# Kernel optimization log

Hardware: AMD Instinct MI355X
Metric: run time of the kernel (lower is better)

The kernel has to match this reference:

```python
import jax, jax.numpy as jnp
import numpy as np

N_ATOMS = 50000
NUM_TYPES = 8
DIM_Q = 64
NUM_NEURONS = 64


def setup_inputs() -> dict:
    key = jax.random.key(0)
    k_q, k_z, k_w0, k_w1 = jax.random.split(key, 4)
    descriptors = jax.random.normal(k_q, (N_ATOMS, DIM_Q), dtype=jnp.float32)
    Z = jax.random.randint(k_z, (N_ATOMS,), 0, NUM_TYPES, dtype=jnp.int32)
    # glorot-ish scaled init for the per-type MLP weights
    W0 = jax.random.normal(k_w0, (NUM_TYPES, DIM_Q, NUM_NEURONS), dtype=jnp.float32) * np.float32(1.0 / np.sqrt(DIM_Q))
    b0 = jnp.zeros((NUM_TYPES, NUM_NEURONS), dtype=jnp.float32)
    W1 = jax.random.normal(k_w1, (NUM_TYPES, NUM_NEURONS), dtype=jnp.float32) * np.float32(1.0 / np.sqrt(NUM_NEURONS))
    b1 = jnp.zeros((), dtype=jnp.float32)
    return {"descriptors": descriptors, "W0": W0, "b0": b0, "W1": W1, "b1": b1, "Z": Z}


def reference(descriptors, W0, b0, W1, b1, Z):
    # Per-type gather of expert weights (the headroom hotspot):
    W0_t = W0[Z]          # [N, dim_q, num_neurons]
    b0_t = b0[Z]          # [N, num_neurons]
    W1_t = W1[Z]          # [N, num_neurons]
    # Batched 1-hidden-layer MLP per atom: h_i = tanh(q_i @ W0[Z_i] + b0[Z_i])
    h = jnp.tanh(jnp.einsum('nd,ndk->nk', descriptors, W0_t) + b0_t)  # [N, num_neurons]
    # Per-atom scalar energy, global bias b1, then total energy (target_mode == 0)
    E_i = jnp.sum(h * W1_t, axis=1) + b1  # [N]
    return jnp.sum(E_i)
```

## Files before the change

### kernel.cpp

```cpp
#include <hip/hip_runtime.h>
#include <math.h>

#define NUM_TYPES 8
#define DIM 64
#define SEG 8192
#define BM 128
#define QS_STRIDE 132

__global__ __launch_bounds__(256) void scatter_kernel(
    const int* __restrict__ Z, int* __restrict__ fill, int* __restrict__ sorted,
    const float* __restrict__ b1, float* __restrict__ out, int N)
{
    __shared__ int cnt[NUM_TYPES];
    __shared__ int base[NUM_TYPES];
    int tid = threadIdx.x;
    if (tid < NUM_TYPES) cnt[tid] = 0;
    __syncthreads();

    int i = blockIdx.x * 256 + tid;
    int z = 0, r = 0;
    bool valid = (i < N);
    if (valid) {
        z = Z[i];
        r = atomicAdd(&cnt[z], 1);
    }
    __syncthreads();
    if (tid < NUM_TYPES) base[tid] = atomicAdd(&fill[tid], cnt[tid]);
    __syncthreads();
    if (valid) {
        int p = base[z] + r;
        if (p < SEG) sorted[z * SEG + p] = i;
    }
    if (i == 0) out[0] = (float)N * b1[0];
}

__global__ __launch_bounds__(256) void mlp_kernel(
    const float* __restrict__ desc, const float* __restrict__ W0,
    const float* __restrict__ b0, const float* __restrict__ W1,
    const int* __restrict__ sorted, const int* __restrict__ fill,
    float* __restrict__ out)
{
    __shared__ float Qs[DIM][QS_STRIDE];
    __shared__ float Ws[DIM][DIM];
    __shared__ int   slots[BM];
    __shared__ float b0s[DIM];
    __shared__ float W1s[DIM];
    __shared__ float wsum[4];

    const int t    = blockIdx.x >> 6;
    const int tile = blockIdx.x & 63;
    const int tid  = threadIdx.x;

    const int cnt_t = fill[t];
    const int a_lo  = tile * BM;
    if (a_lo >= cnt_t) return;

    if (tid < BM)
        slots[tid] = (a_lo + tid < cnt_t) ? sorted[t * SEG + a_lo + tid] : -1;

    {
        const float4* w0v = (const float4*)(W0 + t * DIM * DIM);
        float4* wsv = (float4*)&Ws[0][0];
        #pragma unroll
        for (int i = 0; i < 4; ++i) wsv[tid + i * 256] = w0v[tid + i * 256];
        if (tid < DIM) { b0s[tid] = b0[t * DIM + tid]; W1s[tid] = W1[t * DIM + tid]; }
    }
    __syncthreads();

    #pragma unroll
    for (int it = 0; it < 8; ++it) {
        int f  = tid + it * 256;
        int a  = f >> 4;
        int dv = (f & 15) << 2;
        int idx = slots[a];
        float4 q = (idx >= 0) ? *(const float4*)(desc + (size_t)idx * DIM + dv)
                              : make_float4(0.f, 0.f, 0.f, 0.f);
        Qs[dv + 0][a] = q.x; Qs[dv + 1][a] = q.y;
        Qs[dv + 2][a] = q.z; Qs[dv + 3][a] = q.w;
    }
    __syncthreads();

    const int ag = tid & 15;
    const int kg = tid >> 4;
    const int a0 = ag * 8;
    const int k0 = kg * 4;

    float acc[8][4] = {};
    #pragma unroll 4
    for (int d = 0; d < DIM; ++d) {
        float4 qa = *(const float4*)&Qs[d][a0];
        float4 qb = *(const float4*)&Qs[d][a0 + 4];
        float4 w  = *(const float4*)&Ws[d][k0];
        float q[8] = {qa.x, qa.y, qa.z, qa.w, qb.x, qb.y, qb.z, qb.w};
        #pragma unroll
        for (int i = 0; i < 8; ++i) {
            acc[i][0] += q[i] * w.x;
            acc[i][1] += q[i] * w.y;
            acc[i][2] += q[i] * w.z;
            acc[i][3] += q[i] * w.w;
        }
    }

    float bk[4], wk[4];
    #pragma unroll
    for (int j = 0; j < 4; ++j) { bk[j] = b0s[k0 + j]; wk[j] = W1s[k0 + j]; }

    float e = 0.f;
    #pragma unroll
    for (int i = 0; i < 8; ++i) {
        if (slots[a0 + i] >= 0) {
            float s = 0.f;
            #pragma unroll
            for (int j = 0; j < 4; ++j) {
                float x  = acc[i][j] + bk[j];
                float u  = __expf(2.0f * x);
                float th = 1.0f - __fdividef(2.0f, u + 1.0f);
                s = fmaf(th, wk[j], s);
            }
            e += s;
        }
    }

    #pragma unroll
    for (int o = 32; o > 0; o >>= 1) e += __shfl_down(e, o, 64);
    if ((tid & 63) == 0) wsum[tid >> 6] = e;
    __syncthreads();
    if (tid == 0) atomicAdd(out, wsum[0] + wsum[1] + wsum[2] + wsum[3]);
}

extern "C" void kernel_launch(void* const* d_in, const int* in_sizes, int n_in,
                              void* d_out, int out_size, void* d_ws, size_t ws_size,
                              hipStream_t stream)
{
    const float* desc = (const float*)d_in[0];
    const float* W0   = (const float*)d_in[1];
    const float* b0   = (const float*)d_in[2];
    const float* W1   = (const float*)d_in[3];
    const float* b1   = (const float*)d_in[4];
    const int*   Z    = (const int*)d_in[5];
    const int N = in_sizes[5];

    int* fill   = (int*)d_ws;
    int* sorted = (int*)((char*)d_ws + 64);

    hipMemsetAsync(fill, 0, NUM_TYPES * sizeof(int), stream);

    scatter_kernel<<<(N + 255) / 256, 256, 0, stream>>>(
        Z, fill, sorted, b1, (float*)d_out, N);

    mlp_kernel<<<NUM_TYPES * (SEG / BM), 256, 0, stream>>>(
        desc, W0, b0, W1, sorted, fill, (float*)d_out);
}
```

Before: 88.21 us.

## Fuse sort and per-type MLP into one kernel with all weights in LDS

Drops the scatter/sort pass and per-type tiled GEMM. A single kernel stages all eight types' W0, b0 and W1 into dynamic LDS, and each thread computes one atom's hidden layer directly by indexing its type's weights. This removes a launch, the index workspace and the gather indirection. In exchange it uses about 131 KB of LDS per block, which limits occupancy, and per-thread descriptor loads are strided and uncoalesced.

After: 88.09 us. No clear change (-0.1%).

```diff
diff --git a/kernel.cpp b/kernel.cpp
--- a/kernel.cpp
+++ b/kernel.cpp
@@ -1,125 +1,88 @@
 #include <hip/hip_runtime.h>
 #include <math.h>
 
+
 #define NUM_TYPES 8
 #define DIM 64
-#define SEG 8192
-#define BM 128
-#define QS_STRIDE 132
+#define W_STRIDE 4100
+#define LDS_FLOATS (NUM_TYPES * W_STRIDE + 2 * NUM_TYPES * DIM)
+#define LDS_BYTES  (LDS_FLOATS * 4)
 
-__global__ __launch_bounds__(256) void scatter_kernel(
-    const int* __restrict__ Z, int* __restrict__ fill, int* __restrict__ sorted,
-    const float* __restrict__ b1, float* __restrict__ out, int N)
+__global__ __launch_bounds__(256) void fused_mlp_kernel(
+    const float* __restrict__ desc, const float* __restrict__ W0,
+    const float* __restrict__ b0, const float* __restrict__ W1,
+    const float* __restrict__ b1, const int* __restrict__ Z,
+    float* __restrict__ out, int N)
 {
-    __shared__ int cnt[NUM_TYPES];
-    __shared__ int base[NUM_TYPES];
-    int tid = threadIdx.x;
-    if (tid < NUM_TYPES) cnt[tid] = 0;
+    extern __shared__ float lds[];
+    float* W0s = lds;
+    float* b0s = lds + NUM_TYPES * W_STRIDE;
+    float* W1s = b0s + NUM_TYPES * DIM;
+    __shared__ float wsum[4];
+
+    const int tid = threadIdx.x;
+
+    #pragma unroll
+    for (int t = 0; t < NUM_TYPES; ++t) {
+        float4* dst = (float4*)(W0s + t * W_STRIDE);
+        const float4* src = (const float4*)(W0 + t * DIM * DIM);
+        #pragma unroll
+        for (int it = 0; it < 4; ++it)
+            dst[tid + it * 256] = src[tid + it * 256];
+    }
+    b0s[tid]       = b0[tid];
+    b0s[tid + 256] = b0[tid + 256];
+    W1s[tid]       = W1[tid];
+    W1s[tid + 256] = W1[tid + 256];
     __syncthreads();
 
-    int i = blockIdx.x * 256 + tid;
-    int z = 0, r = 0;
-    bool valid = (i < N);
-    if (valid) {
-        z = Z[i];
-        r = atomicAdd(&cnt[z], 1);
-    }
-    __syncthreads();
-    if (tid < NUM_TYPES) base[tid] = atomicAdd(&fill[tid], cnt[tid]);
-    __syncthreads();
-    if (valid) {
-        int p = base[z] + r;
-        if (p < SEG) sorted[z * SEG + p] = i;
-    }
-    if (i == 0) out[0] = (float)N * b1[0];
-}
+    const int i = blockIdx.x * 256 + tid;
+    float e = 0.0f;
+    if (i < N) {
+        const int z = Z[i];
+        const float4* Wz  = (const float4*)(W0s + z * W_STRIDE);
+        const float4* qv  = (const float4*)(desc + (size_t)i * DIM);
+        const float4* bz  = (const float4*)(b0s + z * DIM);
+        const float4* w1z = (const float4*)(W1s + z * DIM);
 
-__global__ __launch_bounds__(256) void mlp_kernel(
-    const float* __restrict__ desc, const float* __restrict__ W0,
-    const float* __restrict__ b0, const float* __restrict__ W1,
-    const int* __restrict__ sorted, const int* __restrict__ fill,
-    float* __restrict__ out)
-{
-    __shared__ float Qs[DIM][QS_STRIDE];
-    __shared__ float Ws[DIM][DIM];
-    __shared__ int   slots[BM];
-    __shared__ float b0s[DIM];
-    __shared__ float W1s[DIM];
-    __shared__ float wsum[4];
+        float4 h[16];
+        #pragma unroll
+        for (int kq = 0; kq < 16; ++kq) h[kq] = bz[kq];
 
-    const int t    = blockIdx.x >> 6;
-    const int tile = blockIdx.x & 63;
-    const int tid  = threadIdx.x;
+        #pragma unroll 4
+        for (int d4 = 0; d4 < 16; ++d4) {
+            float4 q4 = qv[d4];
+            #pragma unroll
+            for (int dd = 0; dd < 4; ++dd) {
+                float qd = (dd == 0) ? q4.x : (dd == 1) ? q4.y
+                         : (dd == 2) ? q4.z : q4.w;
+                const float4* Wrow = Wz + (d4 * 4 + dd) * 16;
+                #pragma unroll
+                for (int kq = 0; kq < 16; ++kq) {
+                    float4 w = Wrow[kq];
+                    h[kq].x = fmaf(qd, w.x, h[kq].x);
+                    h[kq].y = fmaf(qd, w.y, h[kq].y);
+                    h[kq].z = fmaf(qd, w.z, h[kq].z);
+                    h[kq].w = fmaf(qd, w.w, h[kq].w);
+                }
+            }
+        }
 
-    const int cnt_t = fill[t];
-    const int a_lo  = tile * BM;
-    if (a_lo >= cnt_t) return;
-
-    if (tid < BM)
-        slots[tid] = (a_lo + tid < cnt_t) ? sorted[t * SEG + a_lo + tid] : -1;
-
-    {
-        const float4* w0v = (const float4*)(W0 + t * DIM * DIM);
-        float4* wsv = (float4*)&Ws[0][0];
         #pragma unroll
-        for (int i = 0; i < 4; ++i) wsv[tid + i * 256] = w0v[tid + i * 256];
-        if (tid < DIM) { b0s[tid] = b0[t * DIM + tid]; W1s[tid] = W1[t * DIM + tid]; }
-    }
-    __syncthreads();
-
-    #pragma unroll
-    for (int it = 0; it < 8; ++it) {
-        int f  = tid + it * 256;
-        int a  = f >> 4;
-        int dv = (f & 15) << 2;
-        int idx = slots[a];
-        float4 q = (idx >= 0) ? *(const float4*)(desc + (size_t)idx * DIM + dv)
-                              : make_float4(0.f, 0.f, 0.f, 0.f);
-        Qs[dv + 0][a] = q.x; Qs[dv + 1][a] = q.y;
-        Qs[dv + 2][a] = q.z; Qs[dv + 3][a] = q.w;
-    }
-    __syncthreads();
-
-    const int ag = tid & 15;
-    const int kg = tid >> 4;
-    const int a0 = ag * 8;
-    const int k0 = kg * 4;
-
-    float acc[8][4] = {};
-    #pragma unroll 4
-    for (int d = 0; d < DIM; ++d) {
-        float4 qa = *(const float4*)&Qs[d][a0];
-        float4 qb = *(const float4*)&Qs[d][a0 + 4];
-        float4 w  = *(const float4*)&Ws[d][k0];
-        float q[8] = {qa.x, qa.y, qa.z, qa.w, qb.x, qb.y, qb.z, qb.w};
-        #pragma unroll
-        for (int i = 0; i < 8; ++i) {
-            acc[i][0] += q[i] * w.x;
-            acc[i][1] += q[i] * w.y;
-            acc[i][2] += q[i] * w.z;
-            acc[i][3] += q[i] * w.w;
+        for (int kq = 0; kq < 16; ++kq) {
+            float4 w1 = w1z[kq];
+            float hv[4] = {h[kq].x, h[kq].y, h[kq].z, h[kq].w};
+            float wv[4] = {w1.x, w1.y, w1.z, w1.w};
+            #pragma unroll
+            for (int j = 0; j < 4; ++j) {
+                float u  = __expf(2.0f * hv[j]);
+                float th = 1.0f - __fdividef(2.0f, u + 1.0f);
+                e = fmaf(th, wv[j], e);
+            }
         }
     }
 
-    float bk[4], wk[4];
-    #pragma unroll
-    for (int j = 0; j < 4; ++j) { bk[j] = b0s[k0 + j]; wk[j] = W1s[k0 + j]; }
-
-    float e = 0.f;
-    #pragma unroll
-    for (int i = 0; i < 8; ++i) {
-        if (slots[a0 + i] >= 0) {
-            float s = 0.f;
-            #pragma unroll
-            for (int j = 0; j < 4; ++j) {
-                float x  = acc[i][j] + bk[j];
-                float u  = __expf(2.0f * x);
-                float th = 1.0f - __fdividef(2.0f, u + 1.0f);
-                s = fmaf(th, wk[j], s);
-            }
-            e += s;
-        }
-    }
+    if (blockIdx.x == 0 && tid == 0) e += (float)N * b1[0];
 
     #pragma unroll
     for (int o = 32; o > 0; o >>= 1) e += __shfl_down(e, o, 64);
@@ -140,14 +103,16 @@
     const int*   Z    = (const int*)d_in[5];
     const int N = in_sizes[5];
 
-    int* fill   = (int*)d_ws;
-    int* sorted = (int*)((char*)d_ws + 64);
+    static bool attr_done = false;
+    if (!attr_done) {
+        (void)hipFuncSetAttribute((const void*)fused_mlp_kernel,
+                                  hipFuncAttributeMaxDynamicSharedMemorySize,
+                                  LDS_BYTES);
+        attr_done = true;
+    }
 
-    hipMemsetAsync(fill, 0, NUM_TYPES * sizeof(int), stream);
+    hipMemsetAsync(d_out, 0, sizeof(float), stream);
 
-    scatter_kernel<<<(N + 255) / 256, 256, 0, stream>>>(
-        Z, fill, sorted, b1, (float*)d_out, N);
-
-    mlp_kernel<<<NUM_TYPES * (SEG / BM), 256, 0, stream>>>(
-        desc, W0, b0, W1, sorted, fill, (float*)d_out);
+    fused_mlp_kernel<<<(N + 255) / 256, 256, LDS_BYTES, stream>>>(
+        desc, W0, b0, W1, b1, Z, (float*)d_out, N);
 }
```
